# Optimization experiments

Measured on AMD Instinct MI355X. Metric: run time of the kernel, lower is better.

Reference implementation:

```python
import jax, jax.numpy as jnp
import numpy as np

D_INV = 1024
N_HEADS = 8
D_HEAD = D_INV // N_HEADS
NEG_INF = -1e9  # masked-out logit value (adj_to_attn_mask)


def setup_inputs() -> dict:
    key = jax.random.key(0)
    ks = jax.random.split(key, 7)
    B, Nq, Nkv = 2, 2048, 2048
    v_inv = jax.random.normal(ks[0], (B, Nkv, D_INV), dtype=jnp.float32)
    messages = jax.random.normal(ks[1], (B, Nq, Nkv, N_HEADS), dtype=jnp.float32)
    adj_matrix = jax.random.randint(ks[2], (B, Nq, Nkv), 0, 2, dtype=jnp.int32)
    scale = 1.0 / np.sqrt(D_INV)
    in_w = jax.random.normal(ks[3], (D_INV, D_INV), dtype=jnp.float32) * scale
    in_b = jax.random.normal(ks[4], (D_INV,), dtype=jnp.float32) * 0.01
    out_w = jax.random.normal(ks[5], (D_INV, D_INV), dtype=jnp.float32) * scale
    out_b = jax.random.normal(ks[6], (D_INV,), dtype=jnp.float32) * 0.01
    return {"v_inv": v_inv, "messages": messages, "adj_matrix": adj_matrix,
            "in_w": in_w, "in_b": in_b, "out_w": out_w, "out_b": out_b}


def reference(v_inv, messages, adj_matrix, in_w, in_b, out_w, out_b):
    B, Nq, Nkv, H = messages.shape
    d_head = v_inv.shape[-1] // H
    # in_proj + split heads: [B, Nkv, H, d_head]
    proj = jnp.einsum('bkd,ed->bke', v_inv, in_w) + in_b
    head_feats = proj.reshape(B, Nkv, H, d_head)
    # adjacency -> additive mask, broadcast over heads
    attn_mask = jnp.where(adj_matrix != 0, 0.0, NEG_INF).astype(messages.dtype)
    logits = messages + attn_mask[..., None]            # [B, Nq, Nkv, H]
    attn = jax.nn.softmax(logits, axis=2)               # softmax over N_kv
    # per-head aggregation: [B, Nq, H, d_head]
    attn_out = jnp.einsum('bqkh,bkhd->bqhd', attn, head_feats)
    # L2-norm weight rescale over N_kv: [B, Nq, H]
    weights = jnp.sqrt(jnp.sum(attn * attn, axis=2))
    attn_out = attn_out * weights[..., None]
    attn_out = attn_out.reshape(B, Nq, H * d_head)
    return jnp.einsum('bqe,de->bqd', attn_out, out_w) + out_b
```

## Files before the change

kernel.cpp:

```cpp
#include <hip/hip_runtime.h>
#include <hip/hip_bf16.h>

typedef float f32x4 __attribute__((ext_vector_type(4)));
typedef __bf16 bf16x8 __attribute__((ext_vector_type(8)));

__device__ __forceinline__ unsigned short f2bf(float f) {
    union { float f; unsigned int u; } v; v.f = f;
    unsigned int u = v.u;
    unsigned int r = (u + 0x7fffu + ((u >> 16) & 1u)) >> 16;
    return (unsigned short)r;
}
__device__ __forceinline__ float bf2f(unsigned short u) {
    union { unsigned int u; float f; } v; v.u = ((unsigned int)u) << 16;
    return v.f;
}

__device__ __forceinline__ void block_sync_lgkm() {
    __asm__ __volatile__("" ::: "memory");
    __builtin_amdgcn_s_waitcnt(0xC07F);
    __builtin_amdgcn_s_barrier();
    __asm__ __volatile__("" ::: "memory");
}

__global__ __launch_bounds__(256) void k_cvt(const float* __restrict__ in,
                                             unsigned short* __restrict__ out, int n4) {
    int i = blockIdx.x * 256 + threadIdx.x;
    if (i >= n4) return;
    float4 v = ((const float4*)in)[i];
    ushort4 o;
    o.x = f2bf(v.x); o.y = f2bf(v.y); o.z = f2bf(v.z); o.w = f2bf(v.w);
    ((ushort4*)out)[i] = o;
}

__global__ __launch_bounds__(256, 4) void k_gemm_in(const unsigned short* __restrict__ A,
                                                    const unsigned short* __restrict__ B,
                                                    const float* __restrict__ bias,
                                                    unsigned short* __restrict__ Vfrag) {
    __shared__ __align__(16) unsigned short As[2][128 * 32];
    __shared__ __align__(16) unsigned short Bs[2][64 * 32];
    const int t = threadIdx.x;
    const int wv = t >> 6, lane = t & 63, mr = lane & 15, quad = lane >> 4;
    const int wi = wv >> 1, wj = wv & 1;
    const int m0 = blockIdx.y * 128, n0 = blockIdx.x * 64;

    f32x4 acc[4][2] = {};
    const int ra0 = t >> 2, ra1 = (t >> 2) + 64, rb = t >> 2;
    const int koff = (t & 3) * 8;

    uint4 pa0 = *(const uint4*)(A + (size_t)(m0 + ra0) * 1024 + koff);
    uint4 pa1 = *(const uint4*)(A + (size_t)(m0 + ra1) * 1024 + koff);
    uint4 pb  = *(const uint4*)(B + (size_t)(n0 + rb)  * 1024 + koff);

    for (int kb = 0; kb < 32; kb++) {
        unsigned short* as = As[kb & 1];
        unsigned short* bs = Bs[kb & 1];
        *(uint4*)&as[ra0 * 32 + koff] = pa0;
        *(uint4*)&as[ra1 * 32 + koff] = pa1;
        *(uint4*)&bs[rb  * 32 + koff] = pb;
        if (kb < 31) {
            int kk = (kb + 1) * 32 + koff;
            pa0 = *(const uint4*)(A + (size_t)(m0 + ra0) * 1024 + kk);
            pa1 = *(const uint4*)(A + (size_t)(m0 + ra1) * 1024 + kk);
            pb  = *(const uint4*)(B + (size_t)(n0 + rb)  * 1024 + kk);
        }
        block_sync_lgkm();
        bf16x8 af[4], bf[2];
        #pragma unroll
        for (int i = 0; i < 4; i++)
            af[i] = *(const bf16x8*)&as[(wi * 64 + i * 16 + mr) * 32 + quad * 8];
        #pragma unroll
        for (int j = 0; j < 2; j++)
            bf[j] = *(const bf16x8*)&bs[(wj * 32 + j * 16 + mr) * 32 + quad * 8];
        #pragma unroll
        for (int i = 0; i < 4; i++)
        #pragma unroll
        for (int j = 0; j < 2; j++)
            acc[i][j] = __builtin_amdgcn_mfma_f32_16x16x32_bf16(af[i], bf[j], acc[i][j], 0, 0, 0);
    }
    #pragma unroll
    for (int i = 0; i < 4; i++)
    #pragma unroll
    for (int j = 0; j < 2; j++) {
        int col = n0 + wj * 32 + j * 16 + mr;
        int row0 = m0 + wi * 64 + i * 16 + quad * 4;
        float be = bias[col];
        int h = col >> 7, d = col & 127;
        int bb = row0 >> 11, k = row0 & 2047;
        size_t idx8 = ((((size_t)(bb * 8 + h) * 64 + (k >> 5)) * 8 + (d >> 4)) * 64
                       + ((k >> 3) & 3) * 16 + (d & 15));
        int j0 = (quad & 1) * 4;
        ushort4 pk;
        pk.x = f2bf(acc[i][j][0] + be);
        pk.y = f2bf(acc[i][j][1] + be);
        pk.z = f2bf(acc[i][j][2] + be);
        pk.w = f2bf(acc[i][j][3] + be);
        *(ushort4*)(Vfrag + idx8 * 8 + j0) = pk;
    }
}

__global__ __launch_bounds__(256, 4) void k_gemm_out(const unsigned short* __restrict__ W,
                                                     const unsigned short* __restrict__ AOS,
                                                     const float* __restrict__ bias,
                                                     float* __restrict__ out) {
    __shared__ __align__(16) unsigned short As[2][128 * 32];
    __shared__ __align__(16) unsigned short Bs[2][64 * 32];
    const int t = threadIdx.x;
    const int wv = t >> 6, lane = t & 63, mr = lane & 15, quad = lane >> 4;
    const int wi = wv >> 1, wj = wv & 1;
    const int e0 = blockIdx.y * 128, r0 = blockIdx.x * 64;

    f32x4 acc[4][2] = {};
    const int ra0 = t >> 2, ra1 = (t >> 2) + 64, rb = t >> 2;
    const int koff = (t & 3) * 8;

    uint4 pa0 = *(const uint4*)(W   + (size_t)(e0 + ra0) * 1024 + koff);
    uint4 pa1 = *(const uint4*)(W   + (size_t)(e0 + ra1) * 1024 + koff);
    uint4 pb  = *(const uint4*)(AOS + (size_t)(r0 + rb)  * 1024 + koff);

    for (int kb = 0; kb < 32; kb++) {
        unsigned short* as = As[kb & 1];
        unsigned short* bs = Bs[kb & 1];
        *(uint4*)&as[ra0 * 32 + koff] = pa0;
        *(uint4*)&as[ra1 * 32 + koff] = pa1;
        *(uint4*)&bs[rb  * 32 + koff] = pb;
        if (kb < 31) {
            int kk = (kb + 1) * 32 + koff;
            pa0 = *(const uint4*)(W   + (size_t)(e0 + ra0) * 1024 + kk);
            pa1 = *(const uint4*)(W   + (size_t)(e0 + ra1) * 1024 + kk);
            pb  = *(const uint4*)(AOS + (size_t)(r0 + rb)  * 1024 + kk);
        }
        block_sync_lgkm();
        bf16x8 af[4], bf[2];
        #pragma unroll
        for (int i = 0; i < 4; i++)
            af[i] = *(const bf16x8*)&as[(wi * 64 + i * 16 + mr) * 32 + quad * 8];
        #pragma unroll
        for (int j = 0; j < 2; j++)
            bf[j] = *(const bf16x8*)&bs[(wj * 32 + j * 16 + mr) * 32 + quad * 8];
        #pragma unroll
        for (int i = 0; i < 4; i++)
        #pragma unroll
        for (int j = 0; j < 2; j++)
            acc[i][j] = __builtin_amdgcn_mfma_f32_16x16x32_bf16(af[i], bf[j], acc[i][j], 0, 0, 0);
    }
    #pragma unroll
    for (int i = 0; i < 4; i++)
    #pragma unroll
    for (int j = 0; j < 2; j++) {
        int r_ = r0 + wj * 32 + j * 16 + mr;
        int e_ = e0 + wi * 64 + i * 16 + quad * 4;
        float4 bv = *(const float4*)&bias[e_];
        float4 o;
        o.x = acc[i][j][0] + bv.x;
        o.y = acc[i][j][1] + bv.y;
        o.z = acc[i][j][2] + bv.z;
        o.w = acc[i][j][3] + bv.w;
        *(float4*)&out[(size_t)r_ * 1024 + e_] = o;
    }
}

__global__ __launch_bounds__(512, 4) void k_attn(const float* __restrict__ msg,
                                                 const int* __restrict__ adj,
                                                 const unsigned short* __restrict__ Vfrag,
                                                 unsigned short* __restrict__ Ppart,
                                                 float* __restrict__ Lpart,
                                                 float* __restrict__ Spart) {
    __shared__ __align__(16) unsigned short lds_p[2][4096];

    const int t = threadIdx.x;
    const int b = blockIdx.x >> 7;
    const int q0 = (blockIdx.x & 127) * 16;
    const int ks = blockIdx.y;

    const int wv = t >> 6, lane = t & 63, mr = lane & 15, quad = lane >> 4;
    const int kl = lane >> 1;
    const int h0 = (lane & 1) * 4;
    const int lm0 = wv;

    const float* msg_base = msg + ((size_t)(b * 2048 + q0) * 2048 + ks * 512) * 8;
    const int* adj_base = adj + (size_t)(b * 2048 + q0) * 2048 + ks * 512;
    const unsigned short* vf_base =
        Vfrag + ((((size_t)(b * 8 + wv) * 64 + ks * 16) * 8) * 64 + lane) * 8;

    const float* mp0 = msg_base + (size_t)lm0 * 16384 + kl * 8 + h0;
    const float* mp1 = mp0 + 8 * 16384;
    const int* ap0 = adj_base + lm0 * 2048 + kl;
    const int* ap1 = ap0 + 8 * 2048;

    float4 m0r = *(const float4*)mp0;
    float4 m1r = *(const float4*)mp1;
    int a0r = ap0[0], a1r = ap1[0];
    bf16x8 vfR[8];
    #pragma unroll
    for (int nc = 0; nc < 8; nc++) vfR[nc] = *(const bf16x8*)(vf_base + nc * 512);

    float laccs[2][4] = {}, saccs[2][4] = {};
    f32x4 acc[8] = {};

    const int sr = wv * 4 + quad;
    const int afrag_off = (sr * 16 + (mr ^ (sr & 15))) * 8;

    for (int kb = 0; kb < 16; kb++) {
        unsigned short* pbuf = lds_p[kb & 1];
        float px[2][4] = {{m0r.x, m0r.y, m0r.z, m0r.w}, {m1r.x, m1r.y, m1r.z, m1r.w}};
        int av[2] = {a0r, a1r};
        #pragma unroll
        for (int qi = 0; qi < 2; qi++) {
            #pragma unroll
            for (int hj = 0; hj < 4; hj++) {
                float pe = av[qi] ? __expf(px[qi][hj]) : 0.f;
                laccs[qi][hj] += pe;
                saccs[qi][hj] += pe * pe;
                int s = (h0 + hj) * 4 + (kl >> 3);
                int m = lm0 + qi * 8;
                pbuf[(s * 16 + (m ^ (s & 15))) * 8 + (kl & 7)] = f2bf(pe);
            }
        }
        if (kb < 15) {
            m0r = *(const float4*)(mp0 + (kb + 1) * 256);
            m1r = *(const float4*)(mp1 + (kb + 1) * 256);
            a0r = ap0[(kb + 1) * 32];
            a1r = ap1[(kb + 1) * 32];
        }
        block_sync_lgkm();
        bf16x8 afrag = *(const bf16x8*)&pbuf[afrag_off];
        #pragma unroll
        for (int nc = 0; nc < 8; nc++)
            acc[nc] = __builtin_amdgcn_mfma_f32_16x16x32_bf16(afrag, vfR[nc], acc[nc], 0, 0, 0);
        if (kb < 15) {
            const unsigned short* vp = vf_base + (size_t)(kb + 1) * 4096;
            #pragma unroll
            for (int nc = 0; nc < 8; nc++) vfR[nc] = *(const bf16x8*)(vp + nc * 512);
        }
    }

    #pragma unroll
    for (int qi = 0; qi < 2; qi++)
    #pragma unroll
    for (int hj = 0; hj < 4; hj++) {
        float l = laccs[qi][hj], s = saccs[qi][hj];
        #pragma unroll
        for (int mdist = 2; mdist <= 32; mdist <<= 1) {
            l += __shfl_xor(l, mdist, 64);
            s += __shfl_xor(s, mdist, 64);
        }
        laccs[qi][hj] = l; saccs[qi][hj] = s;
    }
    if (lane < 2) {
        int hbase = lane * 4;
        #pragma unroll
        for (int qi = 0; qi < 2; qi++) {
            size_t ridx = ((size_t)ks * 4096 + b * 2048 + q0 + wv + qi * 8) * 8 + hbase;
            #pragma unroll
            for (int hj = 0; hj < 4; hj++) {
                Lpart[ridx + hj] = laccs[qi][hj];
                Spart[ridx + hj] = saccs[qi][hj];
            }
        }
    }

    size_t cbase = ((((size_t)ks * 256 + blockIdx.x) * 8 + wv) * 8) * 64 + lane;
    #pragma unroll
    for (int nc = 0; nc < 8; nc++) {
        ushort4 pk;
        pk.x = f2bf(acc[nc][0]);
        pk.y = f2bf(acc[nc][1]);
        pk.z = f2bf(acc[nc][2]);
        pk.w = f2bf(acc[nc][3]);
        *(ushort4*)(Ppart + (cbase + (size_t)nc * 64) * 4) = pk;
    }
}

__global__ __launch_bounds__(512) void k_combine(const unsigned short* __restrict__ Ppart,
                                                 const float* __restrict__ Lpart,
                                                 const float* __restrict__ Spart,
                                                 unsigned short* __restrict__ AOS) {
    __shared__ float lds_w[128];
    __shared__ __align__(16) unsigned short lds_t[16 * 1032];
    const int t = threadIdx.x;
    const int bx = blockIdx.x;
    const int b = bx >> 7, q0 = (bx & 127) * 16;

    if (t < 128) {
        int q = t >> 3, h = t & 7;
        float l = 0.f, s2 = 0.f;
        #pragma unroll
        for (int ks = 0; ks < 4; ks++) {
            size_t idx = ((size_t)ks * 4096 + b * 2048 + q0 + q) * 8 + h;
            l += Lpart[idx];
            s2 += Spart[idx];
        }
        lds_w[t] = __fsqrt_rn(s2) / (l * l);
    }
    __syncthreads();
    #pragma unroll
    for (int p = 0; p < 8; p++) {
        int u = p * 512 + t;
        int lane = u & 63, nc = (u >> 6) & 7, wvp = u >> 9;
        int mr = lane & 15, quad = lane >> 4;
        float s[4] = {};
        #pragma unroll
        for (int ks = 0; ks < 4; ks++) {
            ushort4 pk = *(const ushort4*)(Ppart +
                (((((size_t)ks * 256 + bx) * 8 + wvp) * 8 + nc) * 64 + lane) * 4);
            s[0] += bf2f(pk.x); s[1] += bf2f(pk.y); s[2] += bf2f(pk.z); s[3] += bf2f(pk.w);
        }
        int e = wvp * 128 + nc * 16 + mr;
        #pragma unroll
        for (int rix = 0; rix < 4; rix++) {
            int q = quad * 4 + rix;
            lds_t[q * 1032 + e] = f2bf(s[rix] * lds_w[q * 8 + wvp]);
        }
    }
    __syncthreads();
    #pragma unroll
    for (int p = 0; p < 4; p++) {
        int le = (p * 512 + t) * 8;
        int q = le >> 10, e = le & 1023;
        uint4 v = *(const uint4*)&lds_t[q * 1032 + e];
        *(uint4*)(AOS + (size_t)(b * 2048 + q0 + q) * 1024 + e) = v;
    }
}

extern "C" void kernel_launch(void* const* d_in, const int* in_sizes, int n_in,
                              void* d_out, int out_size, void* d_ws, size_t ws_size,
                              hipStream_t stream) {
    const float* v_inv    = (const float*)d_in[0];
    const float* messages = (const float*)d_in[1];
    const int*   adjm     = (const int*)d_in[2];
    const float* in_w     = (const float*)d_in[3];
    const float* in_b     = (const float*)d_in[4];
    const float* out_w    = (const float*)d_in[5];
    const float* out_b    = (const float*)d_in[6];
    float* out = (float*)d_out;

    char* ws = (char*)d_ws;
    unsigned short* vinv_bf = (unsigned short*)(ws);
    unsigned short* inw_bf  = (unsigned short*)(ws + (size_t)(8  << 20));
    unsigned short* outw_bf = (unsigned short*)(ws + (size_t)(10 << 20));
    unsigned short* Vfrag   = (unsigned short*)(ws + (size_t)(12 << 20));
    unsigned short* AOS     = (unsigned short*)(ws + (size_t)(20 << 20));
    unsigned short* Ppart   = (unsigned short*)(ws + (size_t)(28 << 20));
    float*          Lpart   = (float*)(ws + (size_t)(60 << 20));
    float*          Spart   = (float*)(ws + (size_t)(60 << 20) + (512 << 10));

    hipLaunchKernelGGL(k_cvt, dim3(4096), dim3(256), 0, stream, v_inv, vinv_bf, 4194304 / 4);
    hipLaunchKernelGGL(k_cvt, dim3(1024), dim3(256), 0, stream, in_w, inw_bf, 1048576 / 4);
    hipLaunchKernelGGL(k_cvt, dim3(1024), dim3(256), 0, stream, out_w, outw_bf, 1048576 / 4);
    hipLaunchKernelGGL(k_gemm_in, dim3(16, 32), dim3(256), 0, stream, vinv_bf, inw_bf, in_b, Vfrag);
    hipLaunchKernelGGL(k_attn, dim3(256, 4), dim3(512), 0, stream, messages, adjm, Vfrag,
                       Ppart, Lpart, Spart);
    hipLaunchKernelGGL(k_combine, dim3(256), dim3(512), 0, stream, Ppart, Lpart, Spart, AOS);
    hipLaunchKernelGGL(k_gemm_out, dim3(64, 8), dim3(256), 0, stream, outw_bf, AOS, out_b, out);
}
```

Baseline: 478.8 us.

## Drop Nkv split in attention and fuse combine into attention kernel

The attention kernel now processes the full Nkv range per block instead of splitting it four ways, so the partial-output buffers and the separate combine kernel are removed. The normalization weights and the transpose to AOS are done in-kernel through LDS. It also adds an XCD-aware block swizzle and replaces the mask branch with an additive bias before exp. The trade-off is a grid of only 256 blocks, which reduces parallelism and latency hiding on a large GPU.

```diff
diff --git a/kernel.cpp b/kernel.cpp
--- a/kernel.cpp
+++ b/kernel.cpp
@@ -159,28 +159,29 @@
     }
 }
 
-__global__ __launch_bounds__(512, 4) void k_attn(const float* __restrict__ msg,
+__global__ __launch_bounds__(512, 2) void k_attn(const float* __restrict__ msg,
                                                  const int* __restrict__ adj,
                                                  const unsigned short* __restrict__ Vfrag,
-                                                 unsigned short* __restrict__ Ppart,
-                                                 float* __restrict__ Lpart,
-                                                 float* __restrict__ Spart) {
+                                                 unsigned short* __restrict__ AOS) {
     __shared__ __align__(16) unsigned short lds_p[2][4096];
+    __shared__ float lds_w[8][16];
+    __shared__ __align__(16) unsigned short lds_t[16 * 1032];
 
     const int t = threadIdx.x;
-    const int b = blockIdx.x >> 7;
-    const int q0 = (blockIdx.x & 127) * 16;
-    const int ks = blockIdx.y;
+    const int wg = (int)blockIdx.x;
+    const int swz = (wg & 7) * 32 + (wg >> 3);
+    const int b = swz >> 7;
+    const int q0 = (swz & 127) * 16;
 
     const int wv = t >> 6, lane = t & 63, mr = lane & 15, quad = lane >> 4;
     const int kl = lane >> 1;
     const int h0 = (lane & 1) * 4;
     const int lm0 = wv;
 
-    const float* msg_base = msg + ((size_t)(b * 2048 + q0) * 2048 + ks * 512) * 8;
-    const int* adj_base = adj + (size_t)(b * 2048 + q0) * 2048 + ks * 512;
+    const float* msg_base = msg + (size_t)(b * 2048 + q0) * 2048 * 8;
+    const int* adj_base = adj + (size_t)(b * 2048 + q0) * 2048;
     const unsigned short* vf_base =
-        Vfrag + ((((size_t)(b * 8 + wv) * 64 + ks * 16) * 8) * 64 + lane) * 8;
+        Vfrag + (((size_t)(b * 8 + wv) * 64 * 8) * 64 + lane) * 8;
 
     const float* mp0 = msg_base + (size_t)lm0 * 16384 + kl * 8 + h0;
     const float* mp1 = mp0 + 8 * 16384;
@@ -200,23 +201,25 @@
     const int sr = wv * 4 + quad;
     const int afrag_off = (sr * 16 + (mr ^ (sr & 15))) * 8;
 
-    for (int kb = 0; kb < 16; kb++) {
+    for (int kb = 0; kb < 64; kb++) {
         unsigned short* pbuf = lds_p[kb & 1];
         float px[2][4] = {{m0r.x, m0r.y, m0r.z, m0r.w}, {m1r.x, m1r.y, m1r.z, m1r.w}};
-        int av[2] = {a0r, a1r};
+        float bl[2];
+        bl[0] = a0r ? 0.f : -1e30f;
+        bl[1] = a1r ? 0.f : -1e30f;
         #pragma unroll
         for (int qi = 0; qi < 2; qi++) {
             #pragma unroll
             for (int hj = 0; hj < 4; hj++) {
-                float pe = av[qi] ? __expf(px[qi][hj]) : 0.f;
+                float pe = __expf(px[qi][hj] + bl[qi]);
                 laccs[qi][hj] += pe;
-                saccs[qi][hj] += pe * pe;
+                saccs[qi][hj] = fmaf(pe, pe, saccs[qi][hj]);
                 int s = (h0 + hj) * 4 + (kl >> 3);
                 int m = lm0 + qi * 8;
                 pbuf[(s * 16 + (m ^ (s & 15))) * 8 + (kl & 7)] = f2bf(pe);
             }
         }
-        if (kb < 15) {
+        if (kb < 63) {
             m0r = *(const float4*)(mp0 + (kb + 1) * 256);
             m1r = *(const float4*)(mp1 + (kb + 1) * 256);
             a0r = ap0[(kb + 1) * 32];
@@ -227,7 +230,7 @@
         #pragma unroll
         for (int nc = 0; nc < 8; nc++)
             acc[nc] = __builtin_amdgcn_mfma_f32_16x16x32_bf16(afrag, vfR[nc], acc[nc], 0, 0, 0);
-        if (kb < 15) {
+        if (kb < 63) {
             const unsigned short* vp = vf_base + (size_t)(kb + 1) * 4096;
             #pragma unroll
             for (int nc = 0; nc < 8; nc++) vfR[nc] = *(const bf16x8*)(vp + nc * 512);
@@ -247,72 +250,26 @@
         laccs[qi][hj] = l; saccs[qi][hj] = s;
     }
     if (lane < 2) {
-        int hbase = lane * 4;
-        #pragma unroll
-        for (int qi = 0; qi < 2; qi++) {
-            size_t ridx = ((size_t)ks * 4096 + b * 2048 + q0 + wv + qi * 8) * 8 + hbase;
-            #pragma unroll
-            for (int hj = 0; hj < 4; hj++) {
-                Lpart[ridx + hj] = laccs[qi][hj];
-                Spart[ridx + hj] = saccs[qi][hj];
-            }
-        }
-    }
-
-    size_t cbase = ((((size_t)ks * 256 + blockIdx.x) * 8 + wv) * 8) * 64 + lane;
+        #pragma unroll
+        for (int qi = 0; qi < 2; qi++)
+        #pragma unroll
+        for (int hj = 0; hj < 4; hj++) {
+            float l = laccs[qi][hj];
+            lds_w[lane * 4 + hj][wv + qi * 8] = __fsqrt_rn(saccs[qi][hj]) / (l * l);
+        }
+    }
+    block_sync_lgkm();
+
+    float4 wq = *(const float4*)&lds_w[wv][quad * 4];
+    float wqa[4] = {wq.x, wq.y, wq.z, wq.w};
     #pragma unroll
     for (int nc = 0; nc < 8; nc++) {
-        ushort4 pk;
-        pk.x = f2bf(acc[nc][0]);
-        pk.y = f2bf(acc[nc][1]);
-        pk.z = f2bf(acc[nc][2]);
-        pk.w = f2bf(acc[nc][3]);
-        *(ushort4*)(Ppart + (cbase + (size_t)nc * 64) * 4) = pk;
-    }
-}
-
-__global__ __launch_bounds__(512) void k_combine(const unsigned short* __restrict__ Ppart,
-                                                 const float* __restrict__ Lpart,
-                                                 const float* __restrict__ Spart,
-                                                 unsigned short* __restrict__ AOS) {
-    __shared__ float lds_w[128];
-    __shared__ __align__(16) unsigned short lds_t[16 * 1032];
-    const int t = threadIdx.x;
-    const int bx = blockIdx.x;
-    const int b = bx >> 7, q0 = (bx & 127) * 16;
-
-    if (t < 128) {
-        int q = t >> 3, h = t & 7;
-        float l = 0.f, s2 = 0.f;
-        #pragma unroll
-        for (int ks = 0; ks < 4; ks++) {
-            size_t idx = ((size_t)ks * 4096 + b * 2048 + q0 + q) * 8 + h;
-            l += Lpart[idx];
-            s2 += Spart[idx];
-        }
-        lds_w[t] = __fsqrt_rn(s2) / (l * l);
-    }
-    __syncthreads();
-    #pragma unroll
-    for (int p = 0; p < 8; p++) {
-        int u = p * 512 + t;
-        int lane = u & 63, nc = (u >> 6) & 7, wvp = u >> 9;
-        int mr = lane & 15, quad = lane >> 4;
-        float s[4] = {};
-        #pragma unroll
-        for (int ks = 0; ks < 4; ks++) {
-            ushort4 pk = *(const ushort4*)(Ppart +
-                (((((size_t)ks * 256 + bx) * 8 + wvp) * 8 + nc) * 64 + lane) * 4);
-            s[0] += bf2f(pk.x); s[1] += bf2f(pk.y); s[2] += bf2f(pk.z); s[3] += bf2f(pk.w);
-        }
-        int e = wvp * 128 + nc * 16 + mr;
-        #pragma unroll
-        for (int rix = 0; rix < 4; rix++) {
-            int q = quad * 4 + rix;
-            lds_t[q * 1032 + e] = f2bf(s[rix] * lds_w[q * 8 + wvp]);
-        }
-    }
-    __syncthreads();
+        int e = wv * 128 + nc * 16 + mr;
+        #pragma unroll
+        for (int j = 0; j < 4; j++)
+            lds_t[(quad * 4 + j) * 1032 + e] = f2bf(acc[nc][j] * wqa[j]);
+    }
+    block_sync_lgkm();
     #pragma unroll
     for (int p = 0; p < 4; p++) {
         int le = (p * 512 + t) * 8;
@@ -340,16 +297,11 @@
     unsigned short* outw_bf = (unsigned short*)(ws + (size_t)(10 << 20));
     unsigned short* Vfrag   = (unsigned short*)(ws + (size_t)(12 << 20));
     unsigned short* AOS     = (unsigned short*)(ws + (size_t)(20 << 20));
-    unsigned short* Ppart   = (unsigned short*)(ws + (size_t)(28 << 20));
-    float*          Lpart   = (float*)(ws + (size_t)(60 << 20));
-    float*          Spart   = (float*)(ws + (size_t)(60 << 20) + (512 << 10));
 
     hipLaunchKernelGGL(k_cvt, dim3(4096), dim3(256), 0, stream, v_inv, vinv_bf, 4194304 / 4);
     hipLaunchKernelGGL(k_cvt, dim3(1024), dim3(256), 0, stream, in_w, inw_bf, 1048576 / 4);
     hipLaunchKernelGGL(k_cvt, dim3(1024), dim3(256), 0, stream, out_w, outw_bf, 1048576 / 4);
     hipLaunchKernelGGL(k_gemm_in, dim3(16, 32), dim3(256), 0, stream, vinv_bf, inw_bf, in_b, Vfrag);
-    hipLaunchKernelGGL(k_attn, dim3(256, 4), dim3(512), 0, stream, messages, adjm, Vfrag,
-                       Ppart, Lpart, Spart);
-    hipLaunchKernelGGL(k_combine, dim3(256), dim3(512), 0, stream, Ppart, Lpart, Spart, AOS);
+    hipLaunchKernelGGL(k_attn, dim3(256), dim3(512), 0, stream, messages, adjm, Vfrag, AOS);
     hipLaunchKernelGGL(k_gemm_out, dim3(64, 8), dim3(256), 0, stream, outw_bf, AOS, out_b, out);
 }
```

New measurement: 460.9 us. 1.04x faster.
